# Optimization experiments

Hardware: AMD Instinct MI355X
Metric: run time of the kernel (lower is better)

Reference implementation:

```python
import jax, jax.numpy as jnp
import numpy as np

FL = 320       # frame length
FS = 80        # frame shift
ORDER = 16     # poly order (a[0] == 1)
EMPH = 0.97    # pre/de-emphasis coefficient


def setup_inputs() -> dict:
    key = jax.random.key(0)
    k1, k2 = jax.random.split(key)
    B, F = 64, 3000
    L = F * FS  # 240000
    excit = jax.random.normal(k1, (B, L, 1), dtype=jnp.float32) * 0.1
    # LPC coefficients: a[0] = 1, remaining taps small for numerical stability
    rest = jax.random.normal(k2, (B, F, ORDER - 1), dtype=jnp.float32) * (0.3 / (ORDER - 1))
    lpc_coef = jnp.concatenate([jnp.ones((B, F, 1), jnp.float32), rest], axis=-1)
    return {"excit": excit, "lpc_coef": lpc_coef}


def reference(excit, lpc_coef):
    """LPCSynthesisPytorch: AR synthesis recursion followed by de-emphasis.

    excit:    (B, L, 1)
    lpc_coef: (B, F, order), a[0] assumed 1, L = F * FS
    returns:  (B, L, 1)
    """
    B, L, _ = excit.shape
    order = lpc_coef.shape[-1]

    # Per-sample AR taps a[1:], expanded frame->sample, time-major for scan.
    a = jnp.repeat(lpc_coef[:, :, 1:], FS, axis=1)[:, :L]      # (B, L, order-1)
    a_t = jnp.transpose(a, (1, 0, 2))                          # (L, B, order-1)
    e_t = jnp.transpose(excit[..., 0], (1, 0))                 # (L, B)

    def ar_step(buf, inp):
        # buf: (B, order-1) = [x[n-order+1], ..., x[n-1]] (last entry most recent)
        a_n, e_n = inp
        # predicted = sum_k a[k] * x[n-k]; output = excit - predicted
        pre = -jnp.sum(a_n * buf[:, ::-1], axis=-1)
        out = e_n + pre
        buf = jnp.concatenate([buf[:, 1:], out[:, None]], axis=-1)
        return buf, out

    buf0 = jnp.zeros((B, order - 1), dtype=excit.dtype)
    _, y_t = jax.lax.scan(ar_step, buf0, (a_t, e_t))           # (L, B)

    # De-emphasis IIR: z[n] = y[n] + EMPH * z[n-1], z[-1] = 0
    def deemph_step(prev, x):
        cur = x + EMPH * prev
        return cur, cur

    _, z_t = jax.lax.scan(deemph_step, jnp.zeros((B,), excit.dtype), y_t)
    return jnp.transpose(z_t, (1, 0))[..., None]               # (B, L, 1)
```

## Files before the change

kernel.cpp:

```cpp
#include <hip/hip_runtime.h>


namespace {
constexpr int kHS = 40;
constexpr int kF = 3000;
constexpr int kH = 2 * kF;
constexpr int kL = kHS * kH;
constexpr int kL4 = kL / 4;
constexpr int kOrder = 16;
constexpr int kB = 64;
constexpr float kEmph = 0.97f;
constexpr int kThreads = 64;
constexpr int kJunk = 9;
constexpr int kEmitH = kThreads - kJunk;
constexpr int kInSlots = kThreads + 2;
constexpr int kIn4 = kInSlots * 10;
constexpr int kTail = kIn4 - 10 * kThreads;
constexpr int kSlotW = 44;
constexpr int kNT = 2;
constexpr int kCols = 55;
constexpr float kLg97 = -4.3943347e-2f;
constexpr float kR1 = 0.2957118f;
constexpr float kR2 = 0.08744547f;
constexpr float kR3 = 0.02585867f;
constexpr float kR4 = 0.00764671f;
constexpr float kR5 = 0.00226126f;
constexpr float kR6 = 6.6867e-4f;
constexpr float kR7 = 1.9773e-4f;
constexpr float kR8 = 5.8472e-5f;

typedef float vfloat4 __attribute__((ext_vector_type(4)));

__device__ __forceinline__ void lds_fence() {
  __builtin_amdgcn_sched_barrier(0);
  asm volatile("s_waitcnt lgkmcnt(0)" ::: "memory");
  __builtin_amdgcn_sched_barrier(0);
}
}

#define AR_SAMPLE(A, s, e_in, ACC)                                         \
  float ACC;                                                               \
  {                                                                        \
    float t0 = (e_in);                                                     \
    t0 = fmaf(-A[14], x[((s)-15) & 15], t0);                               \
    t0 = fmaf(-A[13], x[((s)-14) & 15], t0);                               \
    t0 = fmaf(-A[12], x[((s)-13) & 15], t0);                               \
    t0 = fmaf(-A[11], x[((s)-12) & 15], t0);                               \
    t0 = fmaf(-A[10], x[((s)-11) & 15], t0);                               \
    float t1 = -A[9] * x[((s)-10) & 15];                                   \
    t1 = fmaf(-A[8], x[((s)-9) & 15], t1);                                 \
    t1 = fmaf(-A[7], x[((s)-8) & 15], t1);                                 \
    t1 = fmaf(-A[6], x[((s)-7) & 15], t1);                                 \
    t1 = fmaf(-A[5], x[((s)-6) & 15], t1);                                 \
    float t2 = -A[4] * x[((s)-5) & 15];                                    \
    t2 = fmaf(-A[3], x[((s)-4) & 15], t2);                                 \
    t2 = fmaf(-A[2], x[((s)-3) & 15], t2);                                 \
    t2 = fmaf(-A[1], x[((s)-2) & 15], t2);                                 \
    const float t01 = t0 + t1;                      \
    t2 = fmaf(-A[0], x[((s)-1) & 15], t2);            \
    ACC = t01 + t2;                                           \
    x[(s)&15] = ACC;                                                       \
  }

#define LOAD_TILE(TILE)                                                    \
  {                                                                        \
    const int base4_ = ((TILE)*kEmitH - 11) * 10;                          \
    _Pragma("unroll") for (int p = 0; p < 11; ++p) {                       \
      const int i_ = min(tid + p * kThreads, kIn4 - 1);                    \
      const int g4_ = min(max(base4_ + i_, 0), kL4 - 1);                   \
      ex[p] = eg[g4_];                                                     \
    }                                                                      \
  }

__global__ __launch_bounds__(kThreads, 3) void lpc_synth_kernel(
    const float* __restrict__ excit, const float* __restrict__ coef,
    float* __restrict__ out) {
  __shared__ float s_x[kInSlots * kSlotW];
  __shared__ float s_zend[kThreads];
  __shared__ float s_zp[kEmitH];

  const int tid = threadIdx.x;
  const int b = blockIdx.y;
  const int tile0 = blockIdx.x * kNT;

  const float* __restrict__ ebase = excit + (size_t)b * kL;
  const float* __restrict__ cbase = coef + (size_t)b * kF * kOrder;
  const vfloat4* __restrict__ eg = (const vfloat4*)ebase;

  vfloat4 ex[11];

  LOAD_TILE(tile0)

#pragma unroll
  for (int t = 0; t < kNT; ++t) {
    const int tile = tile0 + t;
    const int hbase = tile * kEmitH;
    const int ht = hbase + tid - kJunk;
    const int hc = min(max(ht, 0), kH - 1);
    const int hw = min(max(ht - 2, 0), kH - 1);

#pragma unroll
    for (int p = 0; p < 11; ++p) {
      if (p < 10 || tid < kTail) {
        const int i = tid + p * kThreads;
        const int slot = i / 10;
        const int o = i - slot * 10;
        *(vfloat4*)(s_x + slot * kSlotW + o * 4) = ex[p];
      }
    }

    const vfloat4* __restrict__ cp_ =
        (const vfloat4*)(cbase + (size_t)(hw >> 1) * kOrder);
    const vfloat4* __restrict__ cc_ =
        (const vfloat4*)(cbase + (size_t)(hc >> 1) * kOrder);
    const vfloat4 p0 = cp_[0], p1 = cp_[1], p2 = cp_[2], p3 = cp_[3];
    const vfloat4 q0 = cc_[0], q1 = cc_[1], q2 = cc_[2], q3 = cc_[3];
    if (t + 1 < kNT) LOAD_TILE(tile0 + t + 1)

    lds_fence();

    float pa_[15] = {p0.y, p0.z, p0.w, p1.x, p1.y, p1.z, p1.w, p2.x,
                     p2.y, p2.z, p2.w, p3.x, p3.y, p3.z, p3.w};
    const float ca_[15] = {q0.y, q0.z, q0.w, q1.x, q1.y, q1.z, q1.w, q2.x,
                           q2.y, q2.z, q2.w, q3.x, q3.y, q3.z, q3.w};

    float x[16];
#pragma unroll
    for (int i = 0; i < 16; ++i) x[i] = 0.f;

    {
      const float* __restrict__ s2 = s_x + tid * kSlotW;
      const float* __restrict__ s1 = s_x + (tid + 1) * kSlotW;
      const float m2 = (ht >= 2) ? 1.f : 0.f;
      const float m1 = (ht >= 1) ? 1.f : 0.f;
#pragma unroll
      for (int j = 8; j < 10; ++j) {
        const vfloat4 v = *(const vfloat4*)(s2 + 4 * j);
        const float f_[4] = {m2 * v.x, m2 * v.y, m2 * v.z, m2 * v.w};
#pragma unroll
        for (int q = 0; q < 4; ++q) {
          AR_SAMPLE(pa_, 4 * (j - 8) + q, f_[q], acc)
          (void)acc;
        }
      }
      if (ht & 1) {
#pragma unroll
        for (int k = 0; k < 15; ++k) pa_[k] = ca_[k];
      }
#pragma unroll
      for (int j = 0; j < 10; ++j) {
        const vfloat4 v = *(const vfloat4*)(s1 + 4 * j);
        const float f_[4] = {m1 * v.x, m1 * v.y, m1 * v.z, m1 * v.w};
#pragma unroll
        for (int q = 0; q < 4; ++q) {
          AR_SAMPLE(pa_, 8 + 4 * j + q, f_[q], acc)
          (void)acc;
        }
      }
    }
    lds_fence();

    float z = 0.f;
    {
      float* __restrict__ so = s_x + (tid + 2) * kSlotW;
#pragma unroll
      for (int j = 0; j < 10; ++j) {
        const vfloat4 v = *(const vfloat4*)(so + 4 * j);
        vfloat4 zv;
#pragma unroll
        for (int q = 0; q < 4; ++q) {
          AR_SAMPLE(ca_, 48 + 4 * j + q, v[q], acc)
          z = fmaf(kEmph, z, acc);
          if (q == 0) zv.x = z;
          if (q == 1) zv.y = z;
          if (q == 2) zv.z = z;
          if (q == 3) zv.w = z;
        }
        *(vfloat4*)(so + 4 * j) = zv;
      }
    }
    s_zend[tid] = (ht < 0 || ht >= kH) ? 0.f : z;
    lds_fence();

    if (tid < kEmitH) {
      float Zp = s_zend[tid + 8];
      Zp = fmaf(kR1, s_zend[tid + 7], Zp);
      Zp = fmaf(kR2, s_zend[tid + 6], Zp);
      Zp = fmaf(kR3, s_zend[tid + 5], Zp);
      Zp = fmaf(kR4, s_zend[tid + 4], Zp);
      Zp = fmaf(kR5, s_zend[tid + 3], Zp);
      Zp = fmaf(kR6, s_zend[tid + 2], Zp);
      Zp = fmaf(kR7, s_zend[tid + 1], Zp);
      Zp = fmaf(kR8, s_zend[tid + 0], Zp);
      s_zp[tid] = Zp;
    }
    lds_fence();

    {
      const int nv4 = min(kEmitH, kH - hbase) * 10;
      vfloat4* __restrict__ ob =
          (vfloat4*)(out + (size_t)b * kL + (size_t)hbase * kHS);
#pragma unroll 1
      for (int i = tid; i < nv4; i += kThreads) {
        const int k = i / 10;
        const int j = i - 10 * k;
        const vfloat4 h =
            *(const vfloat4*)(s_x + (k + 11) * kSlotW + 4 * j);
        const float Zp = s_zp[k];
        const float ee = __builtin_exp2f(kLg97 * (float)(4 * j + 1));
        vfloat4 v;
        v.x = fmaf(ee, Zp, h.x);
        v.y = fmaf(ee * 0.97f, Zp, h.y);
        v.z = fmaf(ee * 0.9409f, Zp, h.z);
        v.w = fmaf(ee * 0.912673f, Zp, h.w);
        ob[i] = v;
      }
    }
    lds_fence();
  }
}
#undef AR_SAMPLE
#undef LOAD_TILE

extern "C" void kernel_launch(void* const* d_in, const int* in_sizes, int n_in,
                              void* d_out, int out_size, void* d_ws,
                              size_t ws_size, hipStream_t stream) {
  const float* excit = (const float*)d_in[0];
  const float* coef = (const float*)d_in[1];
  float* out = (float*)d_out;

  dim3 grid(kCols, kB);
  lpc_synth_kernel<<<grid, kThreads, 0, stream>>>(excit, coef, out);
}
```

Before: 137.9 us.

## Stage excitation tiles via async global-to-LDS loads with double buffering

Replaces the register-staged excitation loads and LDS writes with `__builtin_amdgcn_global_load_lds` DMA into a double-buffered LDS area. The next tile's data and LPC coefficients are prefetched while the current tile is processed, with a hand-tuned `vmcnt` wait that lets the previous tile's output stores stay in flight. Each block now walks 5 tiles over a 22-column grid with launch bounds of 1 instead of 3. The aim is to hide global load latency and remove the VGPR round trip, at the cost of fewer, longer blocks and a fragile dependence on exact memory-op ordering for correctness.

```diff
diff --git a/kernel.cpp b/kernel.cpp
--- a/kernel.cpp
+++ b/kernel.cpp
@@ -6,19 +6,18 @@
 constexpr int kF = 3000;
 constexpr int kH = 2 * kF;
 constexpr int kL = kHS * kH;
-constexpr int kL4 = kL / 4;
 constexpr int kOrder = 16;
 constexpr int kB = 64;
 constexpr float kEmph = 0.97f;
 constexpr int kThreads = 64;
 constexpr int kJunk = 9;
 constexpr int kEmitH = kThreads - kJunk;
-constexpr int kInSlots = kThreads + 2;
-constexpr int kIn4 = kInSlots * 10;
-constexpr int kTail = kIn4 - 10 * kThreads;
+constexpr int kInSlots = 66;
 constexpr int kSlotW = 44;
-constexpr int kNT = 2;
-constexpr int kCols = 55;
+constexpr int kChunks = 12;
+constexpr int kBufF = kChunks * 256;
+constexpr int kNT = 5;
+constexpr int kCols = 22;
 constexpr float kLg97 = -4.3943347e-2f;
 constexpr float kR1 = 0.2957118f;
 constexpr float kR2 = 0.08744547f;
@@ -35,6 +34,23 @@
   __builtin_amdgcn_sched_barrier(0);
   asm volatile("s_waitcnt lgkmcnt(0)" ::: "memory");
   __builtin_amdgcn_sched_barrier(0);
+}
+
+__device__ __forceinline__ void stage_tile(const float* __restrict__ ebase,
+                                           float* sbuf, int hbase, int ln) {
+#pragma unroll
+  for (int c = 0; c < kChunks; ++c) {
+    const int W4 = c * 64 + ln;
+    const int s = min(W4 / 11, kInSlots - 1);
+    const int o4 = W4 - s * 11;
+    const int hts = hbase + s - 11;
+    const int hcs = min(max(hts, 0), kH - 1);
+    const int fidx = min(hcs * kHS + o4 * 4, kL - 4);
+    __builtin_amdgcn_global_load_lds(
+        (const __attribute__((address_space(1))) float*)(ebase + fidx),
+        (__attribute__((address_space(3))) float*)(sbuf + (c << 8)), 16, 0,
+        0);
+  }
 }
 }
 
@@ -62,20 +78,10 @@
     x[(s)&15] = ACC;                                                       \
   }
 
-#define LOAD_TILE(TILE)                                                    \
-  {                                                                        \
-    const int base4_ = ((TILE)*kEmitH - 11) * 10;                          \
-    _Pragma("unroll") for (int p = 0; p < 11; ++p) {                       \
-      const int i_ = min(tid + p * kThreads, kIn4 - 1);                    \
-      const int g4_ = min(max(base4_ + i_, 0), kL4 - 1);                   \
-      ex[p] = eg[g4_];                                                     \
-    }                                                                      \
-  }
-
-__global__ __launch_bounds__(kThreads, 3) void lpc_synth_kernel(
+__global__ __launch_bounds__(kThreads, 1) void lpc_synth_kernel(
     const float* __restrict__ excit, const float* __restrict__ coef,
     float* __restrict__ out) {
-  __shared__ float s_x[kInSlots * kSlotW];
+  __shared__ float s_ex[2 * kBufF];
   __shared__ float s_zend[kThreads];
   __shared__ float s_zp[kEmitH];
 
@@ -85,39 +91,52 @@
 
   const float* __restrict__ ebase = excit + (size_t)b * kL;
   const float* __restrict__ cbase = coef + (size_t)b * kF * kOrder;
-  const vfloat4* __restrict__ eg = (const vfloat4*)ebase;
-
-  vfloat4 ex[11];
-
-  LOAD_TILE(tile0)
-
-#pragma unroll
+
+  vfloat4 p0, p1, p2, p3, q0, q1, q2, q3;
+  vfloat4 n0, n1, n2, n3, m0, m1v, m2v, m3;
+
+  {
+    const int ht = tile0 * kEmitH + tid - kJunk;
+    const int hc = min(max(ht, 0), kH - 1);
+    const int hw = min(max(ht - 2, 0), kH - 1);
+    const vfloat4* __restrict__ cp_ =
+        (const vfloat4*)(cbase + (size_t)(hw >> 1) * kOrder);
+    const vfloat4* __restrict__ cc_ =
+        (const vfloat4*)(cbase + (size_t)(hc >> 1) * kOrder);
+    p0 = cp_[0]; p1 = cp_[1]; p2 = cp_[2]; p3 = cp_[3];
+    q0 = cc_[0]; q1 = cc_[1]; q2 = cc_[2]; q3 = cc_[3];
+    stage_tile(ebase, s_ex, tile0 * kEmitH, tid);
+  }
+
+#pragma unroll 1
   for (int t = 0; t < kNT; ++t) {
     const int tile = tile0 + t;
     const int hbase = tile * kEmitH;
     const int ht = hbase + tid - kJunk;
-    const int hc = min(max(ht, 0), kH - 1);
-    const int hw = min(max(ht - 2, 0), kH - 1);
-
-#pragma unroll
-    for (int p = 0; p < 11; ++p) {
-      if (p < 10 || tid < kTail) {
-        const int i = tid + p * kThreads;
-        const int slot = i / 10;
-        const int o = i - slot * 10;
-        *(vfloat4*)(s_x + slot * kSlotW + o * 4) = ex[p];
-      }
-    }
-
-    const vfloat4* __restrict__ cp_ =
-        (const vfloat4*)(cbase + (size_t)(hw >> 1) * kOrder);
-    const vfloat4* __restrict__ cc_ =
-        (const vfloat4*)(cbase + (size_t)(hc >> 1) * kOrder);
-    const vfloat4 p0 = cp_[0], p1 = cp_[1], p2 = cp_[2], p3 = cp_[3];
-    const vfloat4 q0 = cc_[0], q1 = cc_[1], q2 = cc_[2], q3 = cc_[3];
-    if (t + 1 < kNT) LOAD_TILE(tile0 + t + 1)
-
-    lds_fence();
+    float* __restrict__ sb = s_ex + (t & 1) * kBufF;
+
+    __builtin_amdgcn_sched_barrier(0);
+    if (t == 0) {
+      asm volatile("s_waitcnt vmcnt(0)" ::: "memory");
+    } else {
+      asm volatile("s_waitcnt vmcnt(9)" ::: "memory");
+    }
+    __builtin_amdgcn_sched_barrier(0);
+
+    if (t + 1 < kNT) {
+      const int htn = (tile + 1) * kEmitH + tid - kJunk;
+      const int hcn = min(max(htn, 0), kH - 1);
+      const int hwn = min(max(htn - 2, 0), kH - 1);
+      const vfloat4* __restrict__ cpn =
+          (const vfloat4*)(cbase + (size_t)(hwn >> 1) * kOrder);
+      const vfloat4* __restrict__ ccn =
+          (const vfloat4*)(cbase + (size_t)(hcn >> 1) * kOrder);
+      n0 = cpn[0]; n1 = cpn[1]; n2 = cpn[2]; n3 = cpn[3];
+      m0 = ccn[0]; m1v = ccn[1]; m2v = ccn[2]; m3 = ccn[3];
+      stage_tile(ebase, s_ex + ((t + 1) & 1) * kBufF,
+                 (tile + 1) * kEmitH, tid);
+    }
+    __builtin_amdgcn_sched_barrier(0);
 
     float pa_[15] = {p0.y, p0.z, p0.w, p1.x, p1.y, p1.z, p1.w, p2.x,
                      p2.y, p2.z, p2.w, p3.x, p3.y, p3.z, p3.w};
@@ -129,14 +148,14 @@
     for (int i = 0; i < 16; ++i) x[i] = 0.f;
 
     {
-      const float* __restrict__ s2 = s_x + tid * kSlotW;
-      const float* __restrict__ s1 = s_x + (tid + 1) * kSlotW;
-      const float m2 = (ht >= 2) ? 1.f : 0.f;
-      const float m1 = (ht >= 1) ? 1.f : 0.f;
+      const float* __restrict__ s2 = sb + tid * kSlotW;
+      const float* __restrict__ s1 = sb + (tid + 1) * kSlotW;
+      const float mm2 = (ht >= 2) ? 1.f : 0.f;
+      const float mm1 = (ht >= 1) ? 1.f : 0.f;
 #pragma unroll
       for (int j = 8; j < 10; ++j) {
         const vfloat4 v = *(const vfloat4*)(s2 + 4 * j);
-        const float f_[4] = {m2 * v.x, m2 * v.y, m2 * v.z, m2 * v.w};
+        const float f_[4] = {mm2 * v.x, mm2 * v.y, mm2 * v.z, mm2 * v.w};
 #pragma unroll
         for (int q = 0; q < 4; ++q) {
           AR_SAMPLE(pa_, 4 * (j - 8) + q, f_[q], acc)
@@ -150,7 +169,7 @@
 #pragma unroll
       for (int j = 0; j < 10; ++j) {
         const vfloat4 v = *(const vfloat4*)(s1 + 4 * j);
-        const float f_[4] = {m1 * v.x, m1 * v.y, m1 * v.z, m1 * v.w};
+        const float f_[4] = {mm1 * v.x, mm1 * v.y, mm1 * v.z, mm1 * v.w};
 #pragma unroll
         for (int q = 0; q < 4; ++q) {
           AR_SAMPLE(pa_, 8 + 4 * j + q, f_[q], acc)
@@ -162,7 +181,7 @@
 
     float z = 0.f;
     {
-      float* __restrict__ so = s_x + (tid + 2) * kSlotW;
+      float* __restrict__ so = sb + (tid + 2) * kSlotW;
 #pragma unroll
       for (int j = 0; j < 10; ++j) {
         const vfloat4 v = *(const vfloat4*)(so + 4 * j);
@@ -204,8 +223,7 @@
       for (int i = tid; i < nv4; i += kThreads) {
         const int k = i / 10;
         const int j = i - 10 * k;
-        const vfloat4 h =
-            *(const vfloat4*)(s_x + (k + 11) * kSlotW + 4 * j);
+        const vfloat4 h = *(const vfloat4*)(sb + (k + 11) * kSlotW + 4 * j);
         const float Zp = s_zp[k];
         const float ee = __builtin_exp2f(kLg97 * (float)(4 * j + 1));
         vfloat4 v;
@@ -217,10 +235,14 @@
       }
     }
     lds_fence();
+
+    if (t + 1 < kNT) {
+      p0 = n0; p1 = n1; p2 = n2; p3 = n3;
+      q0 = m0; q1 = m1v; q2 = m2v; q3 = m3;
+    }
   }
 }
 #undef AR_SAMPLE
-#undef LOAD_TILE
 
 extern "C" void kernel_launch(void* const* d_in, const int* in_sizes, int n_in,
                               void* d_out, int out_size, void* d_ws,
```

Measured after the change: 132.7 us. -3.8%, faster.
